# Kernel tuning notes

Hardware: AMD Instinct MI355X
Metric: run time of the kernel (lower is better)

The kernel has to match this reference:

```python
import jax, jax.numpy as jnp
import numpy as np

# MANO kinematic tree (16 LBS joints): wrist root, 5 fingers x 3 joints
PARENTS = np.array([-1, 0, 1, 2, 0, 4, 5, 0, 7, 8, 0, 10, 11, 0, 13, 14])
B, NV, NJ_LBS, NJ_REG, NCOMPS = 4096, 1084, 16, 21, 45


def rodrigues(r):
    """Axis-angle [N,3] -> rotation matrices [N,3,3]."""
    eps = 1e-8
    angle = jnp.sqrt(jnp.sum(r * r, axis=-1, keepdims=True) + eps)  # [N,1]
    axis = r / angle
    c = jnp.cos(angle)[..., None]  # [N,1,1]
    s = jnp.sin(angle)[..., None]
    x, y, z = axis[:, 0], axis[:, 1], axis[:, 2]
    zeros = jnp.zeros_like(x)
    K = jnp.stack([zeros, -z, y, z, zeros, -x, -y, x, zeros], axis=-1).reshape(-1, 3, 3)
    I = jnp.eye(3, dtype=r.dtype)
    return I + s * K + (1.0 - c) * jnp.matmul(K, K)


def global_rigid_transform(Rs, Js):
    """Rs [B,16,3,3], Js [B,16,3] -> (posed joints [B,16,3], relative transforms A [B,16,4,4])."""
    b = Rs.shape[0]
    bottom = jnp.broadcast_to(jnp.array([0.0, 0.0, 0.0, 1.0], dtype=Rs.dtype), (b, 1, 4))

    def make_A(R, t):  # R [B,3,3], t [B,3] -> [B,4,4]
        top = jnp.concatenate([R, t[..., None]], axis=-1)
        return jnp.concatenate([top, bottom], axis=1)

    results = [make_A(Rs[:, 0], Js[:, 0])]
    for i in range(1, NJ_LBS):  # fixed small loop over kinematic tree
        p = int(PARENTS[i])
        t = Js[:, i] - Js[:, p]
        results.append(jnp.matmul(results[p], make_A(Rs[:, i], t)))
    A_world = jnp.stack(results, axis=1)  # [B,16,4,4]
    new_J = A_world[:, :, :3, 3]
    # A = A_world - pack(A_world @ [J;0])  (remove rest-pose joint translation)
    Jh = jnp.concatenate([Js, jnp.zeros_like(Js[..., :1])], axis=-1)  # [B,16,4]
    init_bone = jnp.einsum('bjpq,bjq->bjp', A_world, Jh)  # [B,16,4]
    A_rel = A_world.at[:, :, :, 3].add(-init_bone)
    return new_J, A_rel


def setup_inputs() -> dict:
    key = jax.random.key(0)
    ks = jax.random.split(key, 8)
    beta = jax.random.normal(ks[0], (B, 10), dtype=jnp.float32)
    theta = jax.random.normal(ks[1], (B, NCOMPS), dtype=jnp.float32)
    wrist_euler = jax.random.normal(ks[2], (B, 3), dtype=jnp.float32) * 0.3
    v_template = jax.random.normal(ks[3], (NV, 3), dtype=jnp.float32) * 0.1
    J_regressor = jax.nn.softmax(jax.random.normal(ks[4], (NV, NJ_REG), dtype=jnp.float32) * 4.0, axis=0)
    hands_comp = jax.random.normal(ks[5], (NCOMPS, 45), dtype=jnp.float32) * 0.05
    hands_mean = jax.random.normal(ks[6], (45,), dtype=jnp.float32) * 0.1
    weights = jax.nn.softmax(jax.random.normal(ks[7], (NV, NJ_LBS), dtype=jnp.float32) * 4.0, axis=1)
    return {"beta": beta, "theta": theta, "wrist_euler": wrist_euler,
            "v_template": v_template, "J_regressor": J_regressor,
            "hands_comp": hands_comp, "hands_mean": hands_mean, "weights": weights}


def reference(beta, theta, wrist_euler, v_template, J_regressor, hands_comp, hands_mean, weights):
    num_batch = beta.shape[0]  # beta only sets batch; forward ignores its values (as in source)
    # rest-pose joints from template: [21,3]
    Jt = jnp.einsum('vc,vj->jc', v_template, J_regressor)
    J = jnp.broadcast_to(Jt[None], (num_batch, NJ_REG, 3))
    # pose_type == 'pca'
    euler_pose = theta @ hands_comp + hands_mean  # [B,45]
    Rs = rodrigues(euler_pose.reshape(-1, 3)).reshape(num_batch, 15, 3, 3)
    global_rot = rodrigues(wrist_euler.reshape(-1, 3)).reshape(num_batch, 1, 3, 3)
    R_all = jnp.concatenate([global_rot, Rs], axis=1)  # [B,16,3,3]
    J_transformed, A = global_rigid_transform(R_all, J[:, :NJ_LBS])
    # linear blend skinning: T = W @ A  -> [B,Nv,4,4]
    W = jnp.broadcast_to(weights[None], (num_batch, NV, NJ_LBS))
    T = jnp.matmul(W, A.reshape(num_batch, NJ_LBS, 16)).reshape(num_batch, NV, 4, 4)
    vh = jnp.concatenate([v_template, jnp.ones_like(v_template[:, :1])], axis=-1)  # [Nv,4]
    verts = jnp.einsum('bvpq,vq->bvp', T, vh)[:, :, :3]  # [B,Nv,3]
    joints = jnp.einsum('bvc,vj->bjc', verts, J_regressor)  # [B,21,3]
    return verts, joints
```

## Files before the change

kernel.cpp:

```cpp
#include <hip/hip_runtime.h>

#define NV 1084
#define NVPAD 1088
#define NPART 64
#define NBATCH 8

typedef __attribute__((ext_vector_type(8))) short short8v;
typedef __attribute__((ext_vector_type(4))) float f32x4;

__device__ inline unsigned short f2bf(float f) {
    unsigned int u = __float_as_uint(f);
    unsigned int r = (u + 0x7FFFu + ((u >> 16) & 1u)) >> 16;
    return (unsigned short)r;
}


__device__ inline void rodrigues9(float x, float y, float z, float R[9]) {
    float n2 = x * x + y * y + z * z + 1e-8f;
    float angle = sqrtf(n2);
    float inv = 1.0f / angle;
    float ax = x * inv, ay = y * inv, az = z * inv;
    float c = cosf(angle), s = sinf(angle);
    float C = 1.0f - c;
    R[0] = 1.0f - C * (ay * ay + az * az);
    R[1] = -s * az + C * ax * ay;
    R[2] = s * ay + C * ax * az;
    R[3] = s * az + C * ax * ay;
    R[4] = 1.0f - C * (ax * ax + az * az);
    R[5] = -s * ax + C * ay * az;
    R[6] = -s * ay + C * ax * az;
    R[7] = s * ax + C * ay * az;
    R[8] = 1.0f - C * (ax * ax + ay * ay);
}

__global__ __launch_bounds__(384) void prep_kernel(
    const float* __restrict__ vt, const float* __restrict__ jreg,
    const float* __restrict__ wts, float* __restrict__ Mpart,
    unsigned short* __restrict__ Gbf) {
    int blk = blockIdx.x;
    int t = threadIdx.x;
    if (blk < NPART) {
        int p = blk;
        int v0 = p * 17, v1 = min(v0 + 17, NV);
        float* mp = Mpart + (size_t)p * 1392;
        if (t < 336) {
            int j = t >> 4, k = t & 15;
            float m0 = 0.f, m1 = 0.f, m2 = 0.f, s = 0.f;
            for (int v = v0; v < v1; ++v) {
                float jw = jreg[v * 21 + j] * wts[v * 16 + k];
                m0 += jw * vt[v * 3 + 0];
                m1 += jw * vt[v * 3 + 1];
                m2 += jw * vt[v * 3 + 2];
                s += jw;
            }
            mp[t * 4 + 0] = m0;
            mp[t * 4 + 1] = m1;
            mp[t * 4 + 2] = m2;
            mp[t * 4 + 3] = s;
        } else if (t < 384) {
            int o = t - 336;
            int j = o / 3, c = o - j * 3;
            float acc = 0.f;
            for (int v = v0; v < v1; ++v) acc += vt[v * 3 + c] * jreg[v * 21 + j];
            mp[1344 + o] = acc;
        }
    } else {
        int idx = (blk - NPART) * 384 + t;
        if (idx < NVPAD * 64) {
            int v = idx >> 6, i = idx & 63;
            int k = i >> 2, d = i & 3;
            float val = 0.f;
            if (v < NV) {
                float vh = (d == 3) ? 1.f : vt[v * 3 + d];
                val = wts[v * 16 + k] * vh;
            }
            Gbf[idx] = f2bf(val);
        }
    }
}

__global__ __launch_bounds__(256) void fk_kernel(
    const float* __restrict__ theta, const float* __restrict__ wrist,
    const float* __restrict__ hc, const float* __restrict__ hm,
    const float* __restrict__ Mpart, float* __restrict__ wsA,
    float* __restrict__ Mfinal, unsigned short* __restrict__ Abf,
    int total, int nFK) {
    int blk = blockIdx.x;
    int t = threadIdx.x;
    if (blk >= nFK) {
        __shared__ float sm[256];
        int q = (blk - nFK) * 64 + (t & 63);
        int pg = t >> 6;
        float acc = 0.f;
#pragma unroll
        for (int u = 0; u < 16; ++u) acc += Mpart[(size_t)(pg * 16 + u) * 1392 + q];
        sm[t] = acc;
        __syncthreads();
        if (pg == 0) Mfinal[q] = sm[t] + sm[t + 64] + sm[t + 128] + sm[t + 192];
        return;
    }
    __shared__ float sred[192];
    __shared__ float sj[48];
    if (t < 192) {
        int g = t / 48, o = t - g * 48;
        float acc = 0.f;
#pragma unroll
        for (int u = 0; u < 16; ++u)
            acc += Mpart[(size_t)(g * 16 + u) * 1392 + 1344 + o];
        sred[t] = acc;
    }
    __syncthreads();
    if (t < 48) sj[t] = sred[t] + sred[48 + t] + sred[96 + t] + sred[144 + t];
    __syncthreads();

    int idx = blk * 256 + t;
    if (idx >= total) return;
    int b = idx / 5, r = idx - b * 5;

    float e[9];
    {
        const float* th = theta + (size_t)b * 45;
        int base = 9 * r;
#pragma unroll
        for (int col = 0; col < 9; ++col) e[col] = hm[base + col];
        for (int k = 0; k < 45; ++k) {
            float tk = th[k];
            const float* hck = hc + k * 45 + base;
#pragma unroll
            for (int col = 0; col < 9; ++col) e[col] += tk * hck[col];
        }
    }

    float R[9];
    rodrigues9(wrist[b * 3 + 0], wrist[b * 3 + 1], wrist[b * 3 + 2], R);
    float J0x = sj[0], J0y = sj[1], J0z = sj[2];
    float Ap[12];
    Ap[0] = R[0]; Ap[1] = R[1]; Ap[2] = R[2]; Ap[3] = J0x;
    Ap[4] = R[3]; Ap[5] = R[4]; Ap[6] = R[5]; Ap[7] = J0y;
    Ap[8] = R[6]; Ap[9] = R[7]; Ap[10] = R[8]; Ap[11] = J0z;
    float* out = wsA + (size_t)b * 192;
    if (r == 0) {
#pragma unroll
        for (int row = 0; row < 3; ++row) {
            float a0 = Ap[row * 4 + 0], a1 = Ap[row * 4 + 1], a2 = Ap[row * 4 + 2];
            float a3 = Ap[row * 4 + 3] - (a0 * J0x + a1 * J0y + a2 * J0z);
            out[row * 4 + 0] = a0;
            out[row * 4 + 1] = a1;
            out[row * 4 + 2] = a2;
            out[row * 4 + 3] = a3;
            ushort4 h;
            h.x = f2bf(a0); h.y = f2bf(a1); h.z = f2bf(a2); h.w = f2bf(a3);
            *(ushort4*)(Abf + (size_t)(3 * b + row) * 64) = h;
        }
    }
    float px = J0x, py = J0y, pz = J0z;
#pragma unroll
    for (int s = 0; s < 3; ++s) {
        int i = r * 3 + s + 1;
        rodrigues9(e[3 * s + 0], e[3 * s + 1], e[3 * s + 2], R);
        float jx = sj[i * 3 + 0], jy = sj[i * 3 + 1], jz = sj[i * 3 + 2];
        float tx = jx - px, ty = jy - py, tz = jz - pz;
        float An[12];
#pragma unroll
        for (int row = 0; row < 3; ++row) {
            An[row * 4 + 0] = Ap[row * 4 + 0] * R[0] + Ap[row * 4 + 1] * R[3] + Ap[row * 4 + 2] * R[6];
            An[row * 4 + 1] = Ap[row * 4 + 0] * R[1] + Ap[row * 4 + 1] * R[4] + Ap[row * 4 + 2] * R[7];
            An[row * 4 + 2] = Ap[row * 4 + 0] * R[2] + Ap[row * 4 + 1] * R[5] + Ap[row * 4 + 2] * R[8];
            An[row * 4 + 3] = Ap[row * 4 + 3] + Ap[row * 4 + 0] * tx + Ap[row * 4 + 1] * ty + Ap[row * 4 + 2] * tz;
        }
        float* oi = out + i * 12;
#pragma unroll
        for (int row = 0; row < 3; ++row) {
            float a0 = An[row * 4 + 0], a1 = An[row * 4 + 1], a2 = An[row * 4 + 2];
            float a3 = An[row * 4 + 3] - (a0 * jx + a1 * jy + a2 * jz);
            oi[row * 4 + 0] = a0;
            oi[row * 4 + 1] = a1;
            oi[row * 4 + 2] = a2;
            oi[row * 4 + 3] = a3;
            ushort4 h;
            h.x = f2bf(a0); h.y = f2bf(a1); h.z = f2bf(a2); h.w = f2bf(a3);
            *(ushort4*)(Abf + (size_t)(3 * b + row) * 64 + 4 * i) = h;
        }
#pragma unroll
        for (int q = 0; q < 12; ++q) Ap[q] = An[q];
        px = jx; py = jy; pz = jz;
    }
}

__global__ __launch_bounds__(256) void verts_joints_kernel(
    const float* __restrict__ wsA, const float* __restrict__ Mfinal,
    const unsigned short* __restrict__ Abf, const unsigned short* __restrict__ Gbf,
    float* __restrict__ verts, float* __restrict__ jout, int nVB) {
    int bid = blockIdx.x;
    int t = threadIdx.x;

    if (bid < nVB) {
        int wv = t >> 6, lane = t & 63;
        int Mblk = bid >> 2, nq = bid & 3;
        int Mbase = Mblk * 64 + wv * 16;
        int lrow = lane & 15, lk = lane >> 4;

        const unsigned short* Ar = Abf + (size_t)(Mbase + lrow) * 64 + lk * 8;
        short8v a0 = *(const short8v*)Ar;
        short8v a1 = *(const short8v*)(Ar + 32);

        int mb = Mbase + lk * 4;
        int base[4];
#pragma unroll
        for (int q = 0; q < 4; ++q) {
            int m = mb + q;
            int bq = m / 3;
            int pq = m - 3 * bq;
            base[q] = bq * (NV * 3) + pq;
        }

        for (int ntl = 0; ntl < 17; ++ntl) {
            int v0 = (nq * 17 + ntl) * 16;
            int v = v0 + lrow;
            const unsigned short* Br = Gbf + (size_t)v * 64 + lk * 8;
            short8v g0 = *(const short8v*)Br;
            short8v g1 = *(const short8v*)(Br + 32);
            f32x4 acc = {0.f, 0.f, 0.f, 0.f};
            acc = __builtin_amdgcn_mfma_f32_16x16x32_bf16(a0, g0, acc, 0, 0, 0);
            acc = __builtin_amdgcn_mfma_f32_16x16x32_bf16(a1, g1, acc, 0, 0, 0);
            if (v < NV) {
                int vo = v * 3;
                verts[base[0] + vo] = acc[0];
                verts[base[1] + vo] = acc[1];
                verts[base[2] + vo] = acc[2];
                verts[base[3] + vo] = acc[3];
            }
        }
    } else {
        int b0 = (bid - nVB) * NBATCH;
        for (int o = t; o < NBATCH * 63; o += 256) {
            int bl = o / 63;
            int rem = o - bl * 63;
            int j = rem / 3;
            int c = rem - j * 3;
            const float* A = wsA + (size_t)(b0 + bl) * 192 + c * 4;
            const float* Mj = Mfinal + j * 64;
            float acc = 0.f;
#pragma unroll
            for (int k = 0; k < 16; ++k) {
                float4 av = *(const float4*)&A[k * 12];
                float4 m = *(const float4*)&Mj[k * 4];
                acc += av.x * m.x + av.y * m.y + av.z * m.z + av.w * m.w;
            }
            jout[(size_t)(b0 + bl) * 63 + rem] = acc;
        }
    }
}

extern "C" void kernel_launch(void* const* d_in, const int* in_sizes, int n_in,
                              void* d_out, int out_size, void* d_ws, size_t ws_size,
                              hipStream_t stream) {
    const float* theta = (const float*)d_in[1];
    const float* wrist = (const float*)d_in[2];
    const float* vtpl  = (const float*)d_in[3];
    const float* jreg  = (const float*)d_in[4];
    const float* hc    = (const float*)d_in[5];
    const float* hm    = (const float*)d_in[6];
    const float* wts   = (const float*)d_in[7];
    int B = in_sizes[1] / 45;

    float* ws     = (float*)d_ws;
    float* wsA    = ws;
    float* Mpart  = ws + (size_t)B * 192;
    float* Mfinal = Mpart + (size_t)NPART * 1392;
    unsigned short* Gbf = (unsigned short*)(Mfinal + 1344);
    unsigned short* Abf = Gbf + (size_t)NVPAD * 64;
    float* verts  = (float*)d_out;
    float* jout   = verts + (size_t)B * NV * 3;

    int nG = (NVPAD * 64 + 383) / 384;
    prep_kernel<<<NPART + nG, 384, 0, stream>>>(vtpl, jreg, wts, Mpart, Gbf);
    int nFK = (B * 5 + 255) / 256;
    fk_kernel<<<nFK + 21, 256, 0, stream>>>(theta, wrist, hc, hm, Mpart, wsA,
                                            Mfinal, Abf, B * 5, nFK);
    int nVB = ((3 * B) / 64) * 4;
    verts_joints_kernel<<<nVB + B / NBATCH, 256, 0, stream>>>(
        wsA, Mfinal, Abf, Gbf, verts, jout, nVB);
}
```

Baseline: 56.95 us.

## Stage vertex MFMA tiles in LDS for coalesced float4 output stores

The vertex kernel now gives each block 16 batches (48 rows) by 64 vertices and gathers the MFMA results into a padded shared-memory tile. The block then writes contiguous float4 chunks of the batch-major verts output, replacing scattered stride-3 scalar stores. This trades more blocks and an extra LDS round trip plus a barrier for coalesced global writes, which dominate this output-bound kernel. A scalar fallback handles the last partial vertex tile.

```diff
diff --git a/kernel.cpp b/kernel.cpp
--- a/kernel.cpp
+++ b/kernel.cpp
@@ -195,40 +195,66 @@
     int t = threadIdx.x;
 
     if (bid < nVB) {
-        int wv = t >> 6, lane = t & 63;
-        int Mblk = bid >> 2, nq = bid & 3;
-        int Mbase = Mblk * 64 + wv * 16;
+        __shared__ float sC[48 * 65];
+        int Mgrp = bid / 17;
+        int vt4 = bid - Mgrp * 17;
+        int v0 = vt4 * 64;
+        int b0 = Mgrp * 16;
+        int w = t >> 6, lane = t & 63;
         int lrow = lane & 15, lk = lane >> 4;
 
-        const unsigned short* Ar = Abf + (size_t)(Mbase + lrow) * 64 + lk * 8;
-        short8v a0 = *(const short8v*)Ar;
-        short8v a1 = *(const short8v*)(Ar + 32);
-
-        int mb = Mbase + lk * 4;
-        int base[4];
-#pragma unroll
-        for (int q = 0; q < 4; ++q) {
-            int m = mb + q;
-            int bq = m / 3;
-            int pq = m - 3 * bq;
-            base[q] = bq * (NV * 3) + pq;
-        }
-
-        for (int ntl = 0; ntl < 17; ++ntl) {
-            int v0 = (nq * 17 + ntl) * 16;
-            int v = v0 + lrow;
-            const unsigned short* Br = Gbf + (size_t)v * 64 + lk * 8;
-            short8v g0 = *(const short8v*)Br;
-            short8v g1 = *(const short8v*)(Br + 32);
+        int v = v0 + w * 16 + lrow;
+        const unsigned short* Br = Gbf + (size_t)v * 64 + lk * 8;
+        short8v g0 = *(const short8v*)Br;
+        short8v g1 = *(const short8v*)(Br + 32);
+
+#pragma unroll
+        for (int msub = 0; msub < 3; ++msub) {
+            const unsigned short* Ar =
+                Abf + (size_t)(Mgrp * 48 + msub * 16 + lrow) * 64 + lk * 8;
+            short8v a0 = *(const short8v*)Ar;
+            short8v a1 = *(const short8v*)(Ar + 32);
             f32x4 acc = {0.f, 0.f, 0.f, 0.f};
             acc = __builtin_amdgcn_mfma_f32_16x16x32_bf16(a0, g0, acc, 0, 0, 0);
             acc = __builtin_amdgcn_mfma_f32_16x16x32_bf16(a1, g1, acc, 0, 0, 0);
-            if (v < NV) {
-                int vo = v * 3;
-                verts[base[0] + vo] = acc[0];
-                verts[base[1] + vo] = acc[1];
-                verts[base[2] + vo] = acc[2];
-                verts[base[3] + vo] = acc[3];
+            float* dst = &sC[(msub * 16 + lk * 4) * 65 + w * 16 + lrow];
+#pragma unroll
+            for (int q = 0; q < 4; ++q) dst[q * 65] = acc[q];
+        }
+        __syncthreads();
+
+        if (v0 + 64 <= NV) {
+#pragma unroll
+            for (int i = 0; i < 3; ++i) {
+                int f = t + 256 * i;
+                int bl = f / 48, r = f - bl * 48;
+                int off = r * 4;
+                float4 val;
+                {
+                    int o0 = off + 0, v_ = o0 / 3, p_ = o0 - v_ * 3;
+                    val.x = sC[(bl * 3 + p_) * 65 + v_];
+                }
+                {
+                    int o1 = off + 1, v_ = o1 / 3, p_ = o1 - v_ * 3;
+                    val.y = sC[(bl * 3 + p_) * 65 + v_];
+                }
+                {
+                    int o2 = off + 2, v_ = o2 / 3, p_ = o2 - v_ * 3;
+                    val.z = sC[(bl * 3 + p_) * 65 + v_];
+                }
+                {
+                    int o3 = off + 3, v_ = o3 / 3, p_ = o3 - v_ * 3;
+                    val.w = sC[(bl * 3 + p_) * 65 + v_];
+                }
+                *(float4*)(verts + (size_t)(b0 + bl) * (NV * 3) + v0 * 3 + off) = val;
+            }
+        } else {
+            int nf = (NV - v0) * 3;
+            for (int e = t; e < 16 * nf; e += 256) {
+                int bl = e / nf, o = e - bl * nf;
+                int v_ = o / 3, p_ = o - v_ * 3;
+                verts[(size_t)(b0 + bl) * (NV * 3) + v0 * 3 + o] =
+                    sC[(bl * 3 + p_) * 65 + v_];
             }
         }
     } else {
@@ -278,7 +304,7 @@
     int nFK = (B * 5 + 255) / 256;
     fk_kernel<<<nFK + 21, 256, 0, stream>>>(theta, wrist, hc, hm, Mpart, wsA,
                                             Mfinal, Abf, B * 5, nFK);
-    int nVB = ((3 * B) / 64) * 4;
+    int nVB = ((3 * B) / 48) * 17;
     verts_joints_kernel<<<nVB + B / NBATCH, 256, 0, stream>>>(
         wsA, Mfinal, Abf, Gbf, verts, jout, nVB);
 }
```

Measured after the change: 57.94 us. Within noise of the previous version (+1.7%).

## Stage verts tile in LDS and emit coalesced nontemporal vector stores

Applied to the files above, without the earlier changes.

Each block now handles 4 batches across all vertices. MFMA results go into a shared-memory tile laid out per (batch,component), and the block then writes contiguous float4 nontemporal stores to the interleaved [B,NV,3] output. This replaces the scattered stride-3 scalar global stores with coalesced writes, at the cost of about 52KB of LDS per block, which lowers occupancy, plus a barrier. The joints output also switches to nontemporal stores.

```diff
diff --git a/kernel.cpp b/kernel.cpp
--- a/kernel.cpp
+++ b/kernel.cpp
@@ -187,6 +187,7 @@
     }
 }
 
+#define SCW 1092
 __global__ __launch_bounds__(256) void verts_joints_kernel(
     const float* __restrict__ wsA, const float* __restrict__ Mfinal,
     const unsigned short* __restrict__ Abf, const unsigned short* __restrict__ Gbf,
@@ -195,41 +196,44 @@
     int t = threadIdx.x;
 
     if (bid < nVB) {
-        int wv = t >> 6, lane = t & 63;
-        int Mblk = bid >> 2, nq = bid & 3;
-        int Mbase = Mblk * 64 + wv * 16;
+        __shared__ float sC[12 * SCW];
+        int b0 = bid * 4;
+        int w = t >> 6, lane = t & 63;
         int lrow = lane & 15, lk = lane >> 4;
 
-        const unsigned short* Ar = Abf + (size_t)(Mbase + lrow) * 64 + lk * 8;
+        const unsigned short* Ar = Abf + (size_t)(b0 * 3 + lrow) * 64 + lk * 8;
         short8v a0 = *(const short8v*)Ar;
         short8v a1 = *(const short8v*)(Ar + 32);
 
-        int mb = Mbase + lk * 4;
-        int base[4];
-#pragma unroll
-        for (int q = 0; q < 4; ++q) {
-            int m = mb + q;
-            int bq = m / 3;
-            int pq = m - 3 * bq;
-            base[q] = bq * (NV * 3) + pq;
-        }
-
-        for (int ntl = 0; ntl < 17; ++ntl) {
-            int v0 = (nq * 17 + ntl) * 16;
-            int v = v0 + lrow;
+        for (int vt4 = w; vt4 < NVPAD / 16; vt4 += 4) {
+            int v = vt4 * 16 + lrow;
             const unsigned short* Br = Gbf + (size_t)v * 64 + lk * 8;
             short8v g0 = *(const short8v*)Br;
             short8v g1 = *(const short8v*)(Br + 32);
             f32x4 acc = {0.f, 0.f, 0.f, 0.f};
             acc = __builtin_amdgcn_mfma_f32_16x16x32_bf16(a0, g0, acc, 0, 0, 0);
             acc = __builtin_amdgcn_mfma_f32_16x16x32_bf16(a1, g1, acc, 0, 0, 0);
-            if (v < NV) {
-                int vo = v * 3;
-                verts[base[0] + vo] = acc[0];
-                verts[base[1] + vo] = acc[1];
-                verts[base[2] + vo] = acc[2];
-                verts[base[3] + vo] = acc[3];
-            }
+            if (lk < 3) {
+                float* dst = &sC[(lk * 4) * SCW + vt4 * 16 + lrow];
+#pragma unroll
+                for (int q = 0; q < 4; ++q) dst[q * SCW] = acc[q];
+            }
+        }
+        __syncthreads();
+
+        float* outp = verts + (size_t)b0 * (NV * 3);
+#pragma unroll 1
+        for (int f = t; f < 3252; f += 256) {
+            int bl = f / 813;
+            int off = (f - bl * 813) * 4;
+            f32x4 val;
+#pragma unroll
+            for (int j = 0; j < 4; ++j) {
+                int o = off + j;
+                int v_ = o / 3, p_ = o - v_ * 3;
+                val[j] = sC[(bl * 3 + p_) * SCW + v_];
+            }
+            __builtin_nontemporal_store(val, (f32x4*)(outp + (size_t)f * 4));
         }
     } else {
         int b0 = (bid - nVB) * NBATCH;
@@ -247,7 +251,7 @@
                 float4 m = *(const float4*)&Mj[k * 4];
                 acc += av.x * m.x + av.y * m.y + av.z * m.z + av.w * m.w;
             }
-            jout[(size_t)(b0 + bl) * 63 + rem] = acc;
+            __builtin_nontemporal_store(acc, jout + (size_t)(b0 + bl) * 63 + rem);
         }
     }
 }
@@ -278,7 +282,7 @@
     int nFK = (B * 5 + 255) / 256;
     fk_kernel<<<nFK + 21, 256, 0, stream>>>(theta, wrist, hc, hm, Mpart, wsA,
                                             Mfinal, Abf, B * 5, nFK);
-    int nVB = ((3 * B) / 64) * 4;
+    int nVB = B / 4;
     verts_joints_kernel<<<nVB + B / NBATCH, 256, 0, stream>>>(
         wsA, Mfinal, Abf, Gbf, verts, jout, nVB);
 }
```

New measurement: 51.84 us. -9.0%, faster.
